# Optimization experiments

Hardware: AMD Instinct MI355X
Metric: run time of the kernel (lower is better)

## Reference

```python
import jax, jax.numpy as jnp
import numpy as np

B, N, D = 4, 2048, 1024
H = 16
HD = D // H


def setup_inputs() -> dict:
    key = jax.random.key(0)
    ks = jax.random.split(key, 6)
    x = jax.random.normal(ks[0], (B, N, D), dtype=jnp.float32)
    # additive causal mask: 0 on/below diagonal, -inf above
    neg = jnp.float32(-1e9)
    causal_mask = jnp.where(jnp.triu(jnp.ones((N, N), dtype=bool), k=1), neg, 0.0).astype(jnp.float32)
    s = 1.0 / np.sqrt(D)
    Wqkv = jax.random.normal(ks[1], (D, 3 * D), dtype=jnp.float32) * s
    bqkv = jax.random.normal(ks[2], (3 * D,), dtype=jnp.float32) * 0.01
    Wproj = jax.random.normal(ks[3], (D, D), dtype=jnp.float32) * s
    bproj = jax.random.normal(ks[4], (D,), dtype=jnp.float32) * 0.01
    return {"x": x, "causal_mask": causal_mask, "Wqkv": Wqkv, "bqkv": bqkv, "Wproj": Wproj, "bproj": bproj}


def reference(x, causal_mask, Wqkv, bqkv, Wproj, bproj):
    b, n, d = x.shape
    qkv = x @ Wqkv + bqkv  # [B,N,3D]
    qkv = qkv.reshape(b, n, 3, H, HD).transpose(2, 0, 3, 1, 4)  # [3,B,H,N,HD]
    q, k, v = qkv[0], qkv[1], qkv[2]
    scale = HD ** -0.5
    attn = jnp.einsum('bhqd,bhkd->bhqk', q, k) * scale  # [B,H,N,N]
    attn = attn + causal_mask  # broadcast [N,N] -> [B,H,N,N]
    attn = jax.nn.softmax(attn, axis=-1)
    out = jnp.einsum('bhqk,bhkd->bhqd', attn, v)  # [B,H,N,HD]
    out = out.transpose(0, 2, 1, 3).reshape(b, n, d)
    return out @ Wproj + bproj
```

## Files before the change

kernel.cpp:

```cpp
#include <hip/hip_runtime.h>
#include <hip/hip_bf16.h>

typedef unsigned short u16;
typedef unsigned int u32;
typedef __attribute__((ext_vector_type(8))) short bf16x8;
typedef __attribute__((ext_vector_type(4))) float f32x4;
typedef __attribute__((ext_vector_type(16))) float f32x16;

#define AS1(p) ((const __attribute__((address_space(1))) void*)(p))
#define AS3(p) ((__attribute__((address_space(3))) void*)(p))
#define STG(src, dst) __builtin_amdgcn_global_load_lds(AS1(src), AS3(dst), 16, 0, 0)

#if __has_builtin(__builtin_amdgcn_exp2f)
#define EXP2F(x) __builtin_amdgcn_exp2f(x)
#else
#define EXP2F(x) exp2f(x)
#endif

static __device__ __forceinline__ float b2f(u16 u) {
  union { unsigned int i; float f; } v; v.i = ((unsigned int)u) << 16; return v.f;
}
static __device__ __forceinline__ u16 f2b(float f) {
  union { float f; unsigned int i; } v; v.f = f;
  unsigned int r = v.i + 0x7FFFu + ((v.i >> 16) & 1u);
  return (u16)(r >> 16);
}
static __device__ __forceinline__ u32 cvt_pk_bf16(float lo, float hi) {
  u32 r;
  asm("v_cvt_pk_bf16_f32 %0, %1, %2" : "=v"(r) : "v"(lo), "v"(hi));
  return r;
}
static __device__ __forceinline__ void permswap(u32& a, u32& b) {
  asm("v_permlane32_swap_b32 %0, %1" : "+v"(a), "+v"(b));
}

__global__ __launch_bounds__(256) void cast_f32_bf16(const float* __restrict__ src,
                                                     u16* __restrict__ dst, int n8) {
  int stride = gridDim.x * blockDim.x;
  for (int i = blockIdx.x * blockDim.x + threadIdx.x; i < n8; i += stride) {
    const float4* s = (const float4*)(src + (size_t)i * 8);
    float4 a = s[0], b = s[1];
    bf16x8 o;
    o[0] = (short)f2b(a.x); o[1] = (short)f2b(a.y); o[2] = (short)f2b(a.z); o[3] = (short)f2b(a.w);
    o[4] = (short)f2b(b.x); o[5] = (short)f2b(b.y); o[6] = (short)f2b(b.z); o[7] = (short)f2b(b.w);
    *(bf16x8*)(dst + (size_t)i * 8) = o;
  }
}

__global__ __launch_bounds__(256) void transpose_w(const float* __restrict__ src,
                                                   u16* __restrict__ dst,
                                                   int R, int C) {
  __shared__ float tile[32][33];
  int c0 = blockIdx.x * 32, r0 = blockIdx.y * 32;
  int tx = threadIdx.x, ty = threadIdx.y;
  for (int i = ty; i < 32; i += 8) tile[i][tx] = src[(size_t)(r0 + i) * C + c0 + tx];
  __syncthreads();
  for (int i = ty; i < 32; i += 8) dst[(size_t)(c0 + i) * R + r0 + tx] = f2b(tile[tx][i]);
}

__global__ __launch_bounds__(256) void transpose_v(const u16* __restrict__ qkv,
                                                   u16* __restrict__ VT) {
  const int N = 2048, TD = 3072, D = 1024;
  int bh = blockIdx.y, n0 = blockIdx.x * 64;
  int b = bh >> 4, h = bh & 15;
  int tid = threadIdx.x;
  __shared__ u16 tl[64][72];
  #pragma unroll
  for (int i = 0; i < 16; ++i) {
    int idx = tid + i * 256;
    int nl = idx >> 6, dd = idx & 63;
    tl[dd][nl] = qkv[(size_t)(b * N + n0 + nl) * TD + 2 * D + h * 64 + dd];
  }
  __syncthreads();
  #pragma unroll
  for (int i = 0; i < 16; ++i) {
    int idx = tid + i * 256;
    int dd = idx >> 6, nl = idx & 63;
    VT[((size_t)bh * 64 + dd) * N + n0 + nl] = tl[dd][nl];
  }
}

template <typename OutT>
__global__ __launch_bounds__(256, 2) void gemm256(
    const u16* __restrict__ A,
    const u16* __restrict__ BT,
    const float* __restrict__ bias,
    OutT* __restrict__ C,
    int M, int N, int K, int nn) {
  __shared__ alignas(16) u16 As[2][256 * 32];
  __shared__ alignas(16) u16 Bs[2][128 * 32];

  const int nwg = gridDim.x, cpx = nwg >> 3, id0 = blockIdx.x;
  const int swz = (id0 & 7) * cpx + (id0 >> 3);
  const int mi = swz / nn, ni = swz % nn;
  const int m0 = mi * 256, n0 = ni * 128;

  const int t = threadIdx.x;
  const int wid = t >> 6, lane = t & 63;
  const int wr = wid >> 1, wc = wid & 1;
  const int rlo = lane & 15, g = lane >> 4;

  const u16* aSrc[4];
  const u16* bSrc[2];
  int dA[4], dB[2];
  #pragma unroll
  for (int k = 0; k < 4; ++k) {
    const int c = t + 256 * k, cs = c ^ ((c >> 3) & 3);
    aSrc[k] = A + (size_t)(m0 + (cs >> 2)) * K + (cs & 3) * 8;
    dA[k] = c * 8;
  }
  #pragma unroll
  for (int k = 0; k < 2; ++k) {
    const int c = t + 256 * k, cs = c ^ ((c >> 3) & 3);
    bSrc[k] = BT + (size_t)(n0 + (cs >> 2)) * K + (cs & 3) * 8;
    dB[k] = c * 8;
  }

  f32x4 acc[8][4] = {};
  const int NT = K >> 5;

  #pragma unroll
  for (int k = 0; k < 4; ++k) STG(aSrc[k], &As[0][dA[k]]);
  #pragma unroll
  for (int k = 0; k < 2; ++k) STG(bSrc[k], &Bs[0][dB[k]]);

  for (int kt = 0; kt < NT; ++kt) {
    const int db = kt & 1;
    __syncthreads();

    if (kt + 1 < NT) {
      const int nx = db ^ 1, ko = (kt + 1) * 32;
      #pragma unroll
      for (int k = 0; k < 4; ++k) STG(aSrc[k] + ko, &As[nx][dA[k]]);
      #pragma unroll
      for (int k = 0; k < 2; ++k) STG(bSrc[k] + ko, &Bs[nx][dB[k]]);
    }

    const char* aB = (const char*)&As[db][0];
    const char* bB = (const char*)&Bs[db][0];
    bf16x8 a[8], b[4];
    #pragma unroll
    for (int fr = 0; fr < 8; ++fr) {
      const int r_ = wr * 128 + fr * 16 + rlo;
      a[fr] = *(const bf16x8*)(aB + (r_ * 64 + ((g ^ ((r_ >> 1) & 3)) << 4)));
    }
    #pragma unroll
    for (int fn = 0; fn < 4; ++fn) {
      const int r_ = wc * 64 + fn * 16 + rlo;
      b[fn] = *(const bf16x8*)(bB + (r_ * 64 + ((g ^ ((r_ >> 1) & 3)) << 4)));
    }
    __builtin_amdgcn_s_setprio(1);
    #pragma unroll
    for (int fr = 0; fr < 8; ++fr)
      #pragma unroll
      for (int fn = 0; fn < 4; ++fn)
        acc[fr][fn] = __builtin_amdgcn_mfma_f32_16x16x32_bf16(a[fr], b[fn], acc[fr][fn], 0, 0, 0);
    __builtin_amdgcn_s_setprio(0);
  }

  #pragma unroll
  for (int fn = 0; fn < 4; ++fn) {
    const int col = n0 + wc * 64 + fn * 16 + rlo;
    const float bv = bias[col];
    #pragma unroll
    for (int fr = 0; fr < 8; ++fr) {
      const int row = m0 + wr * 128 + fr * 16 + g * 4;
      #pragma unroll
      for (int i = 0; i < 4; ++i) {
        float r = acc[fr][fn][i] + bv;
        if constexpr (sizeof(OutT) == 2)
          C[(size_t)(row + i) * N + col] = (OutT)f2b(r);
        else
          C[(size_t)(row + i) * N + col] = (OutT)r;
      }
    }
  }
}

__global__ __launch_bounds__(256, 2) void attn_fwd(
    const u16* __restrict__ qkv,
    const u16* __restrict__ VT,
    u16* __restrict__ O) {
  const int N = 2048, TD = 3072, D = 1024;
  const int bid = blockIdx.x;
  const int qp = bid >> 6, bh = bid & 63;
  const int b = bh >> 4, h = bh & 15;
  const int t = threadIdx.x, w = t >> 6, lane = t & 63;
  const int l31 = lane & 31, hi = lane >> 5;
  const int qh = w >> 1, st = w & 1;

  __shared__ alignas(16) u16 pool16[2][64 * 64];
  __shared__ float rsLds[2][32];
  float* poolf = (float*)&pool16[0][0];

  const int c1 = t, c2 = t + 256;
  const int r1 = c1 >> 3, sc1 = ((c1 & 7) ^ (r1 & 7)) * 8;
  const int r2 = c2 >> 3, sc2 = ((c2 & 7) ^ (r2 & 7)) * 8;
  const u16* kbase = qkv + (size_t)(b * N) * TD + D + h * 64;
  const u16* vbase = VT + (size_t)bh * 64 * N;

  const float L2E = 1.44269504089f;
  const float NSH = -23.0830992f;

  for (int pass = 0; pass < 2; ++pass) {
    const int qt = pass ? (15 - qp) : qp;
    const int qbw = qt * 128 + qh * 64;

    bf16x8 qf[2][4];
    #pragma unroll
    for (int qs = 0; qs < 2; ++qs) {
      const u16* qp_ = qkv + ((size_t)(b * N) + qbw + qs * 32 + l31) * TD + h * 64 + hi * 8;
      #pragma unroll
      for (int c = 0; c < 4; ++c) {
        bf16x8 v = *(const bf16x8*)(qp_ + c * 16);
        #pragma unroll
        for (int j = 0; j < 8; ++j)
          v[j] = (short)f2b(b2f((u16)v[j]) * 0.125f);
        qf[qs][c] = v;
      }
    }

    f32x16 o_acc[2][2] = {};
    float psum[2] = {0.f, 0.f};
    const int jend = qt * 128 + 64;

    for (int j0 = 0; j0 <= jend; j0 += 64) {
      STG(kbase + (size_t)(j0 + r1) * TD + sc1, &pool16[0][c1 * 8]);
      STG(kbase + (size_t)(j0 + r2) * TD + sc2, &pool16[0][c2 * 8]);
      STG(vbase + (size_t)r1 * N + j0 + sc1, &pool16[1][c1 * 8]);
      STG(vbase + (size_t)r2 * N + j0 + sc2, &pool16[1][c2 * 8]);
      __syncthreads();

      const int sb = j0 + st * 32;
      if (sb <= qbw + 63) {
        bf16x8 kf[4];
        {
          const int row = st * 32 + l31, sw = (row & 7) << 3;
          #pragma unroll
          for (int c = 0; c < 4; ++c)
            kf[c] = *(const bf16x8*)&pool16[0][row * 64 + ((c * 16 + hi * 8) ^ sw)];
        }
        bf16x8 vf[2][2];
        #pragma unroll
        for (int dt = 0; dt < 2; ++dt) {
          const int row = dt * 32 + l31, sw = (row & 7) << 3;
          #pragma unroll
          for (int kc = 0; kc < 2; ++kc)
            vf[kc][dt] = *(const bf16x8*)&pool16[1][row * 64 + ((st * 32 + kc * 16 + hi * 8) ^ sw)];
        }

        #pragma unroll
        for (int qs = 0; qs < 2; ++qs) {
          if (qs == 0 && sb > qbw + 31) continue;
          const int qr = qbw + qs * 32 + l31;
          f32x16 S = {};
          __builtin_amdgcn_s_setprio(1);
          #pragma unroll
          for (int c = 0; c < 4; ++c)
            S = __builtin_amdgcn_mfma_f32_32x32x16_bf16(kf[c], qf[qs][c], S, 0, 0, 0);
          __builtin_amdgcn_s_setprio(0);
          if (sb + 31 > qbw + qs * 32) {
            const int kvb = sb + 4 * hi;
            #pragma unroll
            for (int r = 0; r < 16; ++r)
              if (kvb + (r & 3) + 8 * (r >> 2) > qr) S[r] = -1e30f;
          }
          float p[16];
          #pragma unroll
          for (int r = 0; r < 16; ++r) p[r] = EXP2F(fmaf(S[r], L2E, NSH));
          float ps = 0.f;
          #pragma unroll
          for (int r = 0; r < 16; ++r) ps += p[r];
          psum[qs] += ps;
          u32 wq[8];
          #pragma unroll
          for (int i = 0; i < 8; ++i) wq[i] = cvt_pk_bf16(p[2 * i], p[2 * i + 1]);
          permswap(wq[0], wq[2]); permswap(wq[1], wq[3]);
          permswap(wq[4], wq[6]); permswap(wq[5], wq[7]);
          union { u32 u[4]; bf16x8 v; } pa0, pa1;
          pa0.u[0] = wq[0]; pa0.u[1] = wq[1]; pa0.u[2] = wq[2]; pa0.u[3] = wq[3];
          pa1.u[0] = wq[4]; pa1.u[1] = wq[5]; pa1.u[2] = wq[6]; pa1.u[3] = wq[7];
          __builtin_amdgcn_s_setprio(1);
          #pragma unroll
          for (int dt = 0; dt < 2; ++dt) {
            o_acc[qs][dt] = __builtin_amdgcn_mfma_f32_32x32x16_bf16(pa0.v, vf[0][dt], o_acc[qs][dt], 0, 0, 0);
            o_acc[qs][dt] = __builtin_amdgcn_mfma_f32_32x32x16_bf16(pa1.v, vf[1][dt], o_acc[qs][dt], 0, 0, 0);
          }
          __builtin_amdgcn_s_setprio(0);
        }
      }
      __syncthreads();
    }

    float rsown[2];
    #pragma unroll
    for (int qs = 0; qs < 2; ++qs)
      rsown[qs] = psum[qs] + __shfl_xor(psum[qs], 32, 64);

    #pragma unroll
    for (int qs = 0; qs < 2; ++qs) {
      if (st != qs) {
        #pragma unroll
        for (int dt = 0; dt < 2; ++dt)
          #pragma unroll
          for (int r = 0; r < 16; ++r)
            poolf[qh * 2048 + (dt * 16 + r) * 64 + lane] = o_acc[qs][dt][r];
        rsLds[qh][l31] = rsown[qs];
      }
      __syncthreads();
      if (st == qs) {
        const float inv = 1.0f / (rsown[qs] + rsLds[qh][l31]);
        #pragma unroll
        for (int r = 0; r < 16; ++r) {
          const int qrow = (r & 3) + 8 * (r >> 2) + 4 * hi;
          const float invq = __shfl(inv, qrow, 64);
          const int q = qbw + qs * 32 + qrow;
          #pragma unroll
          for (int dt = 0; dt < 2; ++dt) {
            const float val = o_acc[qs][dt][r] + poolf[qh * 2048 + (dt * 16 + r) * 64 + lane];
            O[((size_t)(b * N) + q) * D + h * 64 + dt * 32 + l31] = f2b(val * invq);
          }
        }
      }
      __syncthreads();
    }
  }
}

extern "C" void kernel_launch(void* const* d_in, const int* in_sizes, int n_in,
                              void* d_out, int out_size, void* d_ws, size_t ws_size,
                              hipStream_t stream) {
  const float* x     = (const float*)d_in[0];
  const float* Wqkv  = (const float*)d_in[2];
  const float* bqkv  = (const float*)d_in[3];
  const float* Wproj = (const float*)d_in[4];
  const float* bproj = (const float*)d_in[5];
  float* out = (float*)d_out;

  const int B = 4, N = 2048, D = 1024, H = 16;
  const int BN = B * N;
  const int TD = 3 * D;

  char* ws = (char*)d_ws;
  u16* qkv    = (u16*)(ws);
  u16* vt     = (u16*)(ws + 50331648);
  u16* aout   = (u16*)(ws + 67108864);
  u16* wqkvT  = (u16*)(ws + 83886080);
  u16* wprojT = (u16*)(ws + 90177536);
  u16* xb     = (u16*)(ws + 92274688);

  cast_f32_bf16<<<2048, 256, 0, stream>>>(x, xb, BN * D / 8);
  transpose_w<<<dim3(TD / 32, D / 32), dim3(32, 8), 0, stream>>>(Wqkv, wqkvT, D, TD);
  transpose_w<<<dim3(D / 32, D / 32), dim3(32, 8), 0, stream>>>(Wproj, wprojT, D, D);
  gemm256<u16><<<768, 256, 0, stream>>>(xb, wqkvT, bqkv, qkv, BN, TD, D, 24);
  transpose_v<<<dim3(N / 64, B * H), 256, 0, stream>>>(qkv, vt);
  attn_fwd<<<512, 256, 0, stream>>>(qkv, vt, aout);
  gemm256<float><<<256, 256, 0, stream>>>(aout, wprojT, bproj, out, BN, D, D, 8);
}
```

Baseline: 194.9 us.

## Triple-buffer GEMM LDS staging with explicit vmcnt waits instead of syncthreads

The bf16 GEMM kernel moves from two to three LDS stage buffers and prefetches two K-tiles ahead. The full `__syncthreads` is replaced by raw `s_barrier` plus partial `s_waitcnt vmcnt` counts, so each iteration waits only for the tile it is about to consume rather than draining every outstanding global-to-LDS load. The aim is to keep more memory traffic in flight and hide load latency behind the MFMA work. The cost is more LDS per block (about 72KB), which could limit occupancy, and correctness now depends on the hand-counted vmcnt values. A local variable in the attention kernel is renamed with no functional change.

```diff
diff --git a/kernel.cpp b/kernel.cpp
--- a/kernel.cpp
+++ b/kernel.cpp
@@ -87,8 +87,8 @@
     const float* __restrict__ bias,
     OutT* __restrict__ C,
     int M, int N, int K, int nn) {
-  __shared__ alignas(16) u16 As[2][256 * 32];
-  __shared__ alignas(16) u16 Bs[2][128 * 32];
+  __shared__ alignas(16) u16 As[3][256 * 32];
+  __shared__ alignas(16) u16 Bs[3][128 * 32];
 
   const int nwg = gridDim.x, cpx = nwg >> 3, id0 = blockIdx.x;
   const int swz = (id0 & 7) * cpx + (id0 >> 3);
@@ -123,21 +123,30 @@
   for (int k = 0; k < 4; ++k) STG(aSrc[k], &As[0][dA[k]]);
   #pragma unroll
   for (int k = 0; k < 2; ++k) STG(bSrc[k], &Bs[0][dB[k]]);
-
+  #pragma unroll
+  for (int k = 0; k < 4; ++k) STG(aSrc[k] + 32, &As[1][dA[k]]);
+  #pragma unroll
+  for (int k = 0; k < 2; ++k) STG(bSrc[k] + 32, &Bs[1][dB[k]]);
+
+  int rb = 0, sb = 2;
   for (int kt = 0; kt < NT; ++kt) {
-    const int db = kt & 1;
-    __syncthreads();
-
-    if (kt + 1 < NT) {
-      const int nx = db ^ 1, ko = (kt + 1) * 32;
-      #pragma unroll
-      for (int k = 0; k < 4; ++k) STG(aSrc[k] + ko, &As[nx][dA[k]]);
-      #pragma unroll
-      for (int k = 0; k < 2; ++k) STG(bSrc[k] + ko, &Bs[nx][dB[k]]);
-    }
-
-    const char* aB = (const char*)&As[db][0];
-    const char* bB = (const char*)&Bs[db][0];
+    __builtin_amdgcn_s_barrier();
+
+    if (kt + 2 < NT) {
+      const int ko = (kt + 2) * 32;
+      #pragma unroll
+      for (int k = 0; k < 4; ++k) STG(aSrc[k] + ko, &As[sb][dA[k]]);
+      #pragma unroll
+      for (int k = 0; k < 2; ++k) STG(bSrc[k] + ko, &Bs[sb][dB[k]]);
+    }
+
+    if (kt + 2 < NT)      asm volatile("s_waitcnt vmcnt(12)" ::: "memory");
+    else if (kt + 1 < NT) asm volatile("s_waitcnt vmcnt(6)" ::: "memory");
+    else                  asm volatile("s_waitcnt vmcnt(0)" ::: "memory");
+    __builtin_amdgcn_s_barrier();
+
+    const char* aB = (const char*)&As[rb][0];
+    const char* bB = (const char*)&Bs[rb][0];
     bf16x8 a[8], b[4];
     #pragma unroll
     for (int fr = 0; fr < 8; ++fr) {
@@ -156,6 +165,9 @@
       for (int fn = 0; fn < 4; ++fn)
         acc[fr][fn] = __builtin_amdgcn_mfma_f32_16x16x32_bf16(a[fr], b[fn], acc[fr][fn], 0, 0, 0);
     __builtin_amdgcn_s_setprio(0);
+
+    rb = (rb == 2) ? 0 : rb + 1;
+    sb = (sb == 2) ? 0 : sb + 1;
   }
 
   #pragma unroll
@@ -231,8 +243,8 @@
       STG(vbase + (size_t)r2 * N + j0 + sc2, &pool16[1][c2 * 8]);
       __syncthreads();
 
-      const int sb = j0 + st * 32;
-      if (sb <= qbw + 63) {
+      const int sb2 = j0 + st * 32;
+      if (sb2 <= qbw + 63) {
         bf16x8 kf[4];
         {
           const int row = st * 32 + l31, sw = (row & 7) << 3;
@@ -251,7 +263,7 @@
 
         #pragma unroll
         for (int qs = 0; qs < 2; ++qs) {
-          if (qs == 0 && sb > qbw + 31) continue;
+          if (qs == 0 && sb2 > qbw + 31) continue;
           const int qr = qbw + qs * 32 + l31;
           f32x16 S = {};
           __builtin_amdgcn_s_setprio(1);
@@ -259,8 +271,8 @@
           for (int c = 0; c < 4; ++c)
             S = __builtin_amdgcn_mfma_f32_32x32x16_bf16(kf[c], qf[qs][c], S, 0, 0, 0);
           __builtin_amdgcn_s_setprio(0);
-          if (sb + 31 > qbw + qs * 32) {
-            const int kvb = sb + 4 * hi;
+          if (sb2 + 31 > qbw + qs * 32) {
+            const int kvb = sb2 + 4 * hi;
             #pragma unroll
             for (int r = 0; r < 16; ++r)
               if (kvb + (r & 3) + 8 * (r >> 2) > qr) S[r] = -1e30f;
```

Measured after the change: 195.5 us. Within noise of the previous version (+0.3%).
